# Optimization experiments

Hardware: AMD Instinct MI355X
Metric: run time of the kernel (lower is better)

Reference implementation:

```python
import jax, jax.numpy as jnp
import numpy as np

# Module constants (from init_kwargs + mp_num=8 from the mesh)
D_MODEL = 1024
N_HEAD = 16
D_HEAD = 64
D_ROT = 64
MP = 8
B, S = 2, 2048
LOCAL = N_HEAD * D_HEAD // MP          # 128 : per-mp-shard qkv dim
F_IN = N_HEAD * D_HEAD * 3 + D_MODEL * 8  # 11264 : fused qkv+ff projection width
D_OUT_IN = D_MODEL + 4 * D_MODEL       # 5120 : attn (1024) + glu (4096) into output_proj
LN_EPS = 1e-5


def _rotate_every_two(x):
    # x: [..., d] with d even -> interleaved (-x2, x1)
    x1 = x[..., ::2]
    x2 = x[..., 1::2]
    return jnp.stack((-x2, x1), axis=-1).reshape(*x.shape[:-1], -1)


def _fixed_pos_embedding(seq_len, dim):
    inv_freq = 1.0 / (10000.0 ** (np.arange(0, dim, 2) / dim))
    t = np.einsum('i,j->ij', np.arange(seq_len), inv_freq)  # [S, dim//2]
    return jnp.asarray(np.sin(t), jnp.float32), jnp.asarray(np.cos(t), jnp.float32)


def _apply_rotary(x, sin, cos):
    # x: [B, S, mp, D_ROT]; sin/cos: [S, D_ROT//2]
    sin = jnp.repeat(sin, 2, axis=-1)[-x.shape[-3]:, None, :]  # [S,1,D_ROT]
    cos = jnp.repeat(cos, 2, axis=-1)[-x.shape[-3]:, None, :]
    return x * cos + _rotate_every_two(x) * sin


def setup_inputs() -> dict:
    key = jax.random.key(0)
    ks = jax.random.split(key, 4)
    x = jax.random.normal(ks[0], (B, S, D_MODEL), jnp.float32)
    attn_bias = jnp.zeros((1, S, S), jnp.float32)
    ln_scale = jnp.ones((D_MODEL,), jnp.float32)
    ln_offset = jnp.zeros((D_MODEL,), jnp.float32)
    w_in = jax.random.normal(ks[1], (D_MODEL, F_IN), jnp.float32) / np.sqrt(D_MODEL)
    b_in = jnp.zeros((F_IN,), jnp.float32)
    w_out = jax.random.normal(ks[2], (D_OUT_IN, D_MODEL), jnp.float32) / np.sqrt(D_MODEL)
    b_out = jnp.zeros((D_MODEL,), jnp.float32)
    return {"x": x, "attn_bias": attn_bias, "ln_scale": ln_scale, "ln_offset": ln_offset,
            "w_in": w_in, "b_in": b_in, "w_out": w_out, "b_out": b_out}


def reference(x, attn_bias, ln_scale, ln_offset, w_in, b_in, w_out, b_out):
    b, s, d = x.shape
    # LayerNorm (create_scale=True, create_offset=True, eps=1e-5)
    mu = jnp.mean(x, axis=-1, keepdims=True)
    var = jnp.var(x, axis=-1, keepdims=True)
    h = (x - mu) * jax.lax.rsqrt(var + LN_EPS) * ln_scale + ln_offset
    # fused QKV + FF projection, then mp split: [B,S,mp,F_IN/mp]
    proj = (h @ w_in + b_in).reshape(b, s, MP, -1)
    q, v, k, ff = jnp.split(proj, [LOCAL, 2 * LOCAL, 3 * LOCAL], axis=-1)
    # rotary on the first D_ROT dims of each mp shard (head_split is a shape no-op)
    sin, cos = _fixed_pos_embedding(s, D_ROT)
    q = jnp.concatenate([_apply_rotary(q[..., :D_ROT], sin, cos), q[..., D_ROT:]], axis=-1)
    k = jnp.concatenate([_apply_rotary(k[..., :D_ROT], sin, cos), k[..., D_ROT:]], axis=-1)
    # attention over h=mp shard-heads of dim LOCAL; scaled by sqrt(d_head) per source
    scale = np.sqrt(D_HEAD).astype(x.dtype)
    logits = jnp.einsum('bthd,bThd->bhtT', q, k) / scale  # [B,MP,S,S]
    causal = jnp.tril(jnp.ones((s, s), x.dtype))[None]
    bias = -1e10 * (1.0 - causal) + attn_bias
    weights = jax.nn.softmax(logits + bias, axis=-1)
    attn_vec = jnp.einsum('bhtT,bThd->bthd', weights, v)  # [B,S,MP,LOCAL]
    # GLU FFN (jax.nn.gelu default = tanh approximation, as in source)
    ff_out, ff_gate = jnp.split(ff, 2, axis=-1)
    glu = ff_out * jax.nn.gelu(ff_gate)  # [B,S,MP,4*D_MODEL/MP]
    # output: concat per-shard then flatten -> output_proj
    out = jnp.concatenate([attn_vec, glu], axis=-1).reshape(b, s, -1)  # [B,S,5120]
    return out @ w_out + b_out
```

## Files before the change

kernel.cpp:

```cpp
#include <hip/hip_runtime.h>
#include <stdint.h>

#define B_   2
#define S_   2048
#define DM   1024
#define FIN  11264
#define DOUT 5120
#define NSH  8
#define DH   128
#define ROWS (B_*S_)

typedef __attribute__((ext_vector_type(8))) __bf16 bf16x8;
typedef __attribute__((ext_vector_type(4))) __bf16 bf16x4;
typedef __attribute__((ext_vector_type(4))) float  f32x4;

union U2 { unsigned int u; __bf16 h[2]; };

__device__ __forceinline__ void gload16(const void* g, void* l) {
    __builtin_amdgcn_global_load_lds((const __attribute__((address_space(1))) void*)g,
                                     (__attribute__((address_space(3))) void*)l, 16, 0, 0);
}

__global__ __launch_bounds__(256) void ln_kernel(const float* __restrict__ x,
                                                 const float* __restrict__ sc,
                                                 const float* __restrict__ of,
                                                 __bf16* __restrict__ h) {
    int row = blockIdx.x, t = threadIdx.x;
    const float4 v = *(const float4*)&x[(size_t)row*DM + t*4];
    float s  = v.x + v.y + v.z + v.w;
    float ss = v.x*v.x + v.y*v.y + v.z*v.z + v.w*v.w;
#pragma unroll
    for (int off = 32; off >= 1; off >>= 1) {
        s  += __shfl_xor(s, off);
        ss += __shfl_xor(ss, off);
    }
    __shared__ float rs_[4], rss_[4];
    int wid = t >> 6, lane = t & 63;
    if (lane == 0) { rs_[wid] = s; rss_[wid] = ss; }
    __syncthreads();
    s  = rs_[0] + rs_[1] + rs_[2] + rs_[3];
    ss = rss_[0] + rss_[1] + rss_[2] + rss_[3];
    float mu  = s * (1.f/DM);
    float var = ss * (1.f/DM) - mu*mu;
    float r   = rsqrtf(var + 1e-5f);
    float4 scv = *(const float4*)&sc[t*4];
    float4 ofv = *(const float4*)&of[t*4];
    bf16x4 o;
    o[0] = (__bf16)((v.x-mu)*r*scv.x + ofv.x);
    o[1] = (__bf16)((v.y-mu)*r*scv.y + ofv.y);
    o[2] = (__bf16)((v.z-mu)*r*scv.z + ofv.z);
    o[3] = (__bf16)((v.w-mu)*r*scv.w + ofv.w);
    *(bf16x4*)&h[(size_t)row*DM + t*4] = o;
}

__global__ __launch_bounds__(256) void transpose_kernel(const float* __restrict__ in,
                                                        __bf16* __restrict__ out,
                                                        int R, int C) {
    __shared__ __bf16 tile[64][72];
    int c0 = blockIdx.x * 64, r0 = blockIdx.y * 64;
    int t = threadIdx.x;
#pragma unroll
    for (int it = 0; it < 4; ++it) {
        int flat = it*1024 + t*4;
        int rl = flat >> 6, cl = flat & 63;
        float4 v = *(const float4*)&in[(size_t)(r0+rl)*C + c0 + cl];
        tile[rl][cl+0] = (__bf16)v.x;
        tile[rl][cl+1] = (__bf16)v.y;
        tile[rl][cl+2] = (__bf16)v.z;
        tile[rl][cl+3] = (__bf16)v.w;
    }
    __syncthreads();
#pragma unroll
    for (int it = 0; it < 4; ++it) {
        int flat = it*1024 + t*4;
        int cl = flat >> 6, rl = flat & 63;
        bf16x4 o;
#pragma unroll
        for (int j = 0; j < 4; ++j) o[j] = tile[rl+j][cl];
        *(bf16x4*)&out[(size_t)(c0+cl)*R + r0 + rl] = o;
    }
}

__global__ __launch_bounds__(256) void vtrans_kernel(const __bf16* __restrict__ in,
                                                     __bf16* __restrict__ out) {
    __shared__ __bf16 tile[64*72];
    int d0 = blockIdx.x*64, s0 = blockIdx.y*64;
    size_t base = (size_t)blockIdx.z * (size_t)S_ * DH;
    int t = threadIdx.x;
#pragma unroll
    for (int it = 0; it < 2; ++it) {
        int idx = it*2048 + t*8;
        int sl = idx >> 6, dl = idx & 63;
        bf16x8 v = *(const bf16x8*)&in[base + (size_t)(s0+sl)*DH + d0+dl];
        int ch = ((dl>>3) ^ (sl&7) ^ ((sl>>3)&7)) & 7;
        *(bf16x8*)&tile[sl*72 + ch*8] = v;
    }
    __syncthreads();
#pragma unroll
    for (int it = 0; it < 2; ++it) {
        int idx = it*2048 + t*8;
        int dl = idx >> 6, sl = idx & 63;
        bf16x8 o;
#pragma unroll
        for (int j = 0; j < 8; ++j) {
            int r = sl + j;
            int ch = ((dl>>3) ^ (r&7) ^ ((r>>3)&7)) & 7;
            o[j] = tile[r*72 + ch*8 + (dl&7)];
        }
        *(bf16x8*)&out[base + (size_t)(d0+dl)*S_ + s0 + sl] = o;
    }
}

#define MFMA4(ACCI, BN) \
    acc[ACCI][BN] = __builtin_amdgcn_mfma_f32_16x16x32_bf16(a[(ACCI)&3][0], b[BN][0], acc[ACCI][BN],0,0,0); \
    acc[ACCI][BN] = __builtin_amdgcn_mfma_f32_16x16x32_bf16(a[(ACCI)&3][1], b[BN][1], acc[ACCI][BN],0,0,0);

__global__ __launch_bounds__(512, 2) void gemm256_kernel(const __bf16* __restrict__ A,
                                                         const __bf16* __restrict__ BT,
                                                         const float* __restrict__ bias,
                                                         __bf16* __restrict__ Cb,
                                                         float* __restrict__ Cf,
                                                         int M, int N, int K, int klen) {
    __shared__ __align__(16) char lds[131072];
    int t = threadIdx.x, wid = t >> 6, lane = t & 63;
    int wr = wid >> 2, wc = wid & 3;
    int fr = lane & 15, fq = lane >> 4;
    int kbeg = blockIdx.z * klen;
    int nbx = gridDim.x;
    int bid = blockIdx.y * nbx + blockIdx.x;
    int cpx = (nbx * gridDim.y) >> 3;
    int swz = (bid & 7) * cpx + (bid >> 3);
    int bx = swz % nbx, by = swz / nbx;
    int m0 = by * 256, n0 = bx * 256;

    const __bf16* srcA[4];
    const __bf16* srcB[4];
#pragma unroll
    for (int j = 0; j < 4; ++j) {
        int F = (j*512 + t) * 16;
        int lr = F >> 7, c = (F & 127) ^ ((lr & 7) << 4);
        srcA[j] = A + (size_t)(m0 + lr) * K + kbeg + (c >> 1);
        int row = ((lr >> 5) & 3) * 64 + (lr >> 7) * 32 + (lr & 31);
        srcB[j] = BT + (size_t)(n0 + row) * K + kbeg + (c >> 1);
    }
    int lrAlo[4], lrAhi[4], lrB[4];
#pragma unroll
    for (int i = 0; i < 4; ++i) {
        lrAlo[i] = (wr*128 + i*16 + fr) * 128;
        lrAhi[i] = lrAlo[i] + 64*128;
    }
#pragma unroll
    for (int n = 0; n < 4; ++n)
        lrB[n] = ((n >> 1)*128 + wc*32 + (n & 1)*16 + fr) * 128;
    int swzb = (fr & 7) << 4;
    int cb00 = (fq*16) ^ swzb;
    int cb01 = (64 + fq*16) ^ swzb;

    f32x4 acc[8][4] = {};
    gload16(srcA[0], lds +     0 + wid*1024);
    gload16(srcA[2], lds + 16384 + wid*1024);
    gload16(srcB[0], lds + 32768 + wid*1024);
    gload16(srcB[1], lds + 40960 + wid*1024);
    gload16(srcB[2], lds + 49152 + wid*1024);
    gload16(srcB[3], lds + 57344 + wid*1024);
    gload16(srcA[1], lds +  8192 + wid*1024);
    gload16(srcA[3], lds + 24576 + wid*1024);
    asm volatile("s_waitcnt vmcnt(4)" ::: "memory");
    __builtin_amdgcn_s_barrier();

    int nit = klen >> 6;
    for (int it = 0; it < nit; ++it) {
        const char* bc = lds + (it & 1) * 65536;
        char* bn = lds + ((it & 1) ^ 1) * 65536;
        const char* bcB = bc + 32768;
        int koff = (it + 1) << 6;
        bool pf = (it + 1 < nit);
        bf16x8 a[4][2], b[4][2];
#pragma unroll
        for (int i = 0; i < 4; ++i) {
            a[i][0] = *(const bf16x8*)(bc + lrAlo[i] + cb00);
            a[i][1] = *(const bf16x8*)(bc + lrAlo[i] + cb01);
        }
        b[0][0] = *(const bf16x8*)(bcB + lrB[0] + cb00);
        b[0][1] = *(const bf16x8*)(bcB + lrB[0] + cb01);
        b[1][0] = *(const bf16x8*)(bcB + lrB[1] + cb00);
        b[1][1] = *(const bf16x8*)(bcB + lrB[1] + cb01);
        if (pf) {
            gload16(srcA[0] + koff, bn +     0 + wid*1024);
            gload16(srcA[2] + koff, bn + 16384 + wid*1024);
            gload16(srcB[0] + koff, bn + 32768 + wid*1024);
            gload16(srcB[1] + koff, bn + 40960 + wid*1024);
            gload16(srcB[2] + koff, bn + 49152 + wid*1024);
            gload16(srcB[3] + koff, bn + 57344 + wid*1024);
            gload16(srcA[1] + koff, bn +  8192 + wid*1024);
            gload16(srcA[3] + koff, bn + 24576 + wid*1024);
        }
        __builtin_amdgcn_s_setprio(1);
#pragma unroll
        for (int i = 0; i < 4; ++i) { MFMA4(i,0) MFMA4(i,1) }
        __builtin_amdgcn_s_setprio(0);
        if (pf) asm volatile("s_waitcnt vmcnt(10)" ::: "memory");
        else    asm volatile("s_waitcnt vmcnt(2)" ::: "memory");
        __builtin_amdgcn_s_barrier();
        b[2][0] = *(const bf16x8*)(bcB + lrB[2] + cb00);
        b[2][1] = *(const bf16x8*)(bcB + lrB[2] + cb01);
        b[3][0] = *(const bf16x8*)(bcB + lrB[3] + cb00);
        b[3][1] = *(const bf16x8*)(bcB + lrB[3] + cb01);
        __builtin_amdgcn_s_setprio(1);
#pragma unroll
        for (int i = 0; i < 4; ++i) { MFMA4(i,2) MFMA4(i,3) }
        __builtin_amdgcn_s_setprio(0);
        if (pf) asm volatile("s_waitcnt vmcnt(8)" ::: "memory");
        else    asm volatile("s_waitcnt vmcnt(0)" ::: "memory");
        __builtin_amdgcn_s_barrier();
#pragma unroll
        for (int i = 0; i < 4; ++i) {
            a[i][0] = *(const bf16x8*)(bc + lrAhi[i] + cb00);
            a[i][1] = *(const bf16x8*)(bc + lrAhi[i] + cb01);
        }
        __builtin_amdgcn_s_setprio(1);
#pragma unroll
        for (int i = 0; i < 4; ++i) { MFMA4(4+i,0) MFMA4(4+i,1) MFMA4(4+i,2) MFMA4(4+i,3) }
        __builtin_amdgcn_s_setprio(0);
        if (pf) {
            asm volatile("s_waitcnt vmcnt(4)" ::: "memory");
            __builtin_amdgcn_s_barrier();
        }
    }
    if (Cb) {
#pragma unroll
        for (int i = 0; i < 8; ++i)
#pragma unroll
            for (int n = 0; n < 4; ++n) {
                int col = n0 + wc*64 + (n >> 1)*32 + (n & 1)*16 + fr;
                float bv = bias[col];
#pragma unroll
                for (int r = 0; r < 4; ++r) {
                    int row = m0 + wr*128 + i*16 + fq*4 + r;
                    Cb[(size_t)row*N + col] = (__bf16)(acc[i][n][r] + bv);
                }
            }
    } else {
        float* Cz = Cf + (size_t)blockIdx.z * M * N;
#pragma unroll
        for (int i = 0; i < 8; ++i)
#pragma unroll
            for (int n = 0; n < 4; ++n) {
                int col = n0 + wc*64 + (n >> 1)*32 + (n & 1)*16 + fr;
#pragma unroll
                for (int r = 0; r < 4; ++r) {
                    int row = m0 + wr*128 + i*16 + fq*4 + r;
                    Cz[(size_t)row*N + col] = acc[i][n][r];
                }
            }
    }
}

__global__ __launch_bounds__(256) void addbias_kernel(const float* __restrict__ pk,
                                                      const float* __restrict__ bias,
                                                      float* __restrict__ out) {
    int idx = blockIdx.x * 256 + threadIdx.x;
    const size_t stride = (size_t)ROWS * DM / 4;
    float4 a0 = ((const float4*)pk)[idx];
    float4 a1 = ((const float4*)pk)[idx + stride];
    float4 a2 = ((const float4*)pk)[idx + 2*stride];
    float4 a3 = ((const float4*)pk)[idx + 3*stride];
    float4 bb = ((const float4*)bias)[idx & 255];
    float4 o;
    o.x = a0.x + a1.x + a2.x + a3.x + bb.x;
    o.y = a0.y + a1.y + a2.y + a3.y + bb.y;
    o.z = a0.z + a1.z + a2.z + a3.z + bb.z;
    o.w = a0.w + a1.w + a2.w + a3.w + bb.w;
    ((float4*)out)[idx] = o;
}

__global__ __launch_bounds__(256) void qkv_rope_kernel(const __bf16* __restrict__ proj,
                                                       __bf16* __restrict__ qh,
                                                       __bf16* __restrict__ kh,
                                                       __bf16* __restrict__ vh) {
    int idx = blockIdx.x * 256 + threadIdx.x;
    int i   = idx & 63;
    int p   = (idx >> 6) & 7;
    int row = idx >> 9;
    int s   = row & (S_ - 1);
    int b   = row >> 11;
    const __bf16* base = proj + (size_t)row*FIN + p*1408;
    int d0 = i*2;
    U2 uq, uv, uk;
    uq.u = *(const unsigned int*)&base[d0];
    uv.u = *(const unsigned int*)&base[128+d0];
    uk.u = *(const unsigned int*)&base[256+d0];
    float q0 = uq.h[0], q1 = uq.h[1];
    float v0 = uv.h[0], v1 = uv.h[1];
    float k0 = uk.h[0], k1 = uk.h[1];
    if (d0 < 64) {
        float inv = exp2f(-(float)i * 0.4152410118609203f);
        float ang = (float)s * inv;
        float cn = __cosf(ang), sn = __sinf(ang);
        float a;
        a = q0*cn - q1*sn; q1 = q1*cn + q0*sn; q0 = a;
        a = k0*cn - k1*sn; k1 = k1*cn + k0*sn; k0 = a;
    }
    size_t o = ((size_t)((b*NSH + p)*S_ + s))*DH + d0;
    U2 oq, ok, ov;
    oq.h[0] = (__bf16)(q0*0.125f); oq.h[1] = (__bf16)(q1*0.125f);
    ok.h[0] = (__bf16)k0;          ok.h[1] = (__bf16)k1;
    ov.h[0] = (__bf16)v0;          ov.h[1] = (__bf16)v1;
    *(unsigned int*)&qh[o] = oq.u;
    *(unsigned int*)&kh[o] = ok.u;
    *(unsigned int*)&vh[o] = ov.u;
}

__global__ __launch_bounds__(256) void glu_kernel(const __bf16* __restrict__ proj,
                                                  __bf16* __restrict__ ag) {
    int idx = blockIdx.x * 256 + threadIdx.x;
    int j2  = (idx & 255) * 2;
    int p   = (idx >> 8) & 7;
    int row = idx >> 11;
    const __bf16* bp = proj + (size_t)row*FIN + p*1408;
    U2 xo, xg, o;
    xo.u = *(const unsigned int*)&bp[384 + j2];
    xg.u = *(const unsigned int*)&bp[896 + j2];
#pragma unroll
    for (int j = 0; j < 2; ++j) {
        float g = xg.h[j];
        float e2 = __expf(1.5957691216057308f*(g + 0.044715f*g*g*g));
        float gl = g * (1.f - 1.f/(e2 + 1.f));
        o.h[j] = (__bf16)((float)xo.h[j] * gl);
    }
    *(unsigned int*)&ag[(size_t)row*DOUT + p*640 + 128 + j2] = o.u;
}

__device__ __forceinline__ void stage_kv(const __bf16* Kb, const __bf16* Vg,
                                         char* KsB, char* VsB,
                                         int kvbase, int t, int wid) {
#pragma unroll
    for (int j = 0; j < 4; ++j) {
        int F = (j*256 + t)*16;
        int r = F >> 8, c = F & 255;
        gload16(Kb + (size_t)(kvbase + r)*DH + ((c ^ ((r & 7) << 4)) >> 1),
                KsB + j*4096 + (wid << 10));
    }
#pragma unroll
    for (int j = 0; j < 4; ++j) {
        int F = (j*256 + t)*16;
        int r = F >> 7, c = F & 127;
        gload16(Vg + (size_t)r*S_ + kvbase + ((c ^ ((r & 7) << 4)) >> 1),
                VsB + j*4096 + (wid << 10));
    }
}

__global__ __launch_bounds__(256, 2) void attn_kernel(const __bf16* __restrict__ qh,
                                                      const __bf16* __restrict__ kh,
                                                      const __bf16* __restrict__ vt,
                                                      const float* __restrict__ ab,
                                                      __bf16* __restrict__ ag) {
    __shared__ __bf16 Ks[2*8192];
    __shared__ __bf16 Vs[2*8192];
    __shared__ __bf16 Ps[4][16*72];
    int bh = blockIdx.y;
    int b = bh >> 3, hh = bh & 7;
    int xr = blockIdx.x;
    int qb = (xr & 1) ? (31 - (xr >> 1)) : (xr >> 1);
    int q0 = qb * 64;
    int t = threadIdx.x, wid = t >> 6, lane = t & 63;
    int fr = lane & 15, fkb = (lane >> 4) * 16;
    const __bf16* Qb = qh + (size_t)bh * S_ * DH;
    const __bf16* Kb = kh + (size_t)bh * S_ * DH;
    const __bf16* Vg = vt + (size_t)bh * DH * S_;
    bf16x8 qf[4];
#pragma unroll
    for (int kk = 0; kk < 4; ++kk)
        qf[kk] = *(const bf16x8*)&Qb[(size_t)(q0 + wid*16 + fr)*DH + kk*32 + (lane>>4)*8];
    float m[4] = {-3e38f, -3e38f, -3e38f, -3e38f};
    float l[4] = {0.f, 0.f, 0.f, 0.f};
    f32x4 o[8] = {};
    int rowb = q0 + wid*16 + (lane >> 4)*4;
    int nit = qb + 1;
    stage_kv(Kb, Vg, (char*)Ks, (char*)Vs, 0, t, wid);
    for (int it = 0; it < nit; ++it) {
        int kv0 = it * 64, cur = it & 1;
        float abv[4][4];
#pragma unroll
        for (int n = 0; n < 4; ++n)
#pragma unroll
            for (int r = 0; r < 4; ++r)
                abv[n][r] = ab[(size_t)(rowb + r)*S_ + kv0 + n*16 + fr];
        if (it + 1 < nit) {
            stage_kv(Kb, Vg, (char*)Ks + (cur^1)*16384, (char*)Vs + (cur^1)*16384,
                     kv0 + 64, t, wid);
            asm volatile("s_waitcnt vmcnt(8)" ::: "memory");
        } else {
            asm volatile("s_waitcnt vmcnt(0)" ::: "memory");
        }
        __builtin_amdgcn_s_barrier();
        const char* KsC = (const char*)Ks + cur*16384;
        float pv[4][4];
        __builtin_amdgcn_s_setprio(1);
#pragma unroll
        for (int n = 0; n < 4; ++n) {
            f32x4 sacc = {};
#pragma unroll
            for (int kk = 0; kk < 4; ++kk) {
                int row = n*16 + fr;
                int c2 = (kk*64 + fkb) ^ ((fr & 7) << 4);
                bf16x8 kf = *(const bf16x8*)(KsC + row*256 + c2);
                sacc = __builtin_amdgcn_mfma_f32_16x16x32_bf16(qf[kk], kf, sacc, 0, 0, 0);
            }
#pragma unroll
            for (int r = 0; r < 4; ++r) pv[n][r] = sacc[r];
        }
        __builtin_amdgcn_s_setprio(0);
#pragma unroll
        for (int n = 0; n < 4; ++n) {
            int col = kv0 + n*16 + fr;
#pragma unroll
            for (int r = 0; r < 4; ++r)
                pv[n][r] += abv[n][r] + (col <= rowb + r ? 0.f : -1e10f);
        }
        float alpha[4];
#pragma unroll
        for (int r = 0; r < 4; ++r) {
            float mx = fmaxf(fmaxf(pv[0][r], pv[1][r]), fmaxf(pv[2][r], pv[3][r]));
#pragma unroll
            for (int off = 8; off >= 1; off >>= 1) mx = fmaxf(mx, __shfl_xor(mx, off));
            float mn = fmaxf(m[r], mx);
            alpha[r] = __expf(m[r] - mn);
            m[r] = mn;
            float sum = 0.f;
#pragma unroll
            for (int n = 0; n < 4; ++n) { pv[n][r] = __expf(pv[n][r] - mn); sum += pv[n][r]; }
#pragma unroll
            for (int off = 8; off >= 1; off >>= 1) sum += __shfl_xor(sum, off);
            l[r] = l[r]*alpha[r] + sum;
        }
#pragma unroll
        for (int nf = 0; nf < 8; ++nf)
#pragma unroll
            for (int r = 0; r < 4; ++r) o[nf][r] *= alpha[r];
#pragma unroll
        for (int n = 0; n < 4; ++n)
#pragma unroll
            for (int r = 0; r < 4; ++r)
                Ps[wid][((lane >> 4)*4 + r)*72 + n*16 + fr] = (__bf16)pv[n][r];
        asm volatile("s_waitcnt lgkmcnt(0)" ::: "memory");
        __builtin_amdgcn_sched_barrier(0);
        bf16x8 pf[2];
#pragma unroll
        for (int kk = 0; kk < 2; ++kk)
            pf[kk] = *(const bf16x8*)&Ps[wid][fr*72 + kk*32 + (lane>>4)*8];
        const char* VsC = (const char*)Vs + cur*16384;
        __builtin_amdgcn_s_setprio(1);
#pragma unroll
        for (int nf = 0; nf < 8; ++nf) {
#pragma unroll
            for (int kk = 0; kk < 2; ++kk) {
                int row = nf*16 + fr;
                int c2 = (kk*64 + fkb) ^ ((fr & 7) << 4);
                bf16x8 vf = *(const bf16x8*)(VsC + row*128 + c2);
                o[nf] = __builtin_amdgcn_mfma_f32_16x16x32_bf16(pf[kk], vf, o[nf], 0, 0, 0);
            }
        }
        __builtin_amdgcn_s_setprio(0);
        asm volatile("s_waitcnt lgkmcnt(0)" ::: "memory");
        __builtin_amdgcn_sched_barrier(0);
        __builtin_amdgcn_s_barrier();
    }
    int rq = (lane >> 4) * 4;
#pragma unroll
    for (int r = 0; r < 4; ++r) {
        float inv = 1.f / l[r];
#pragma unroll
        for (int nf = 0; nf < 8; ++nf) {
            int qr = q0 + wid*16 + rq + r;
            int d = nf*16 + fr;
            ag[((size_t)(b*S_ + qr))*DOUT + hh*640 + d] = (__bf16)(o[nf][r] * inv);
        }
    }
}

extern "C" void kernel_launch(void* const* d_in, const int* in_sizes, int n_in,
                              void* d_out, int out_size, void* d_ws, size_t ws_size,
                              hipStream_t stream) {
    const float* x     = (const float*)d_in[0];
    const float* ab    = (const float*)d_in[1];
    const float* lns   = (const float*)d_in[2];
    const float* lno   = (const float*)d_in[3];
    const float* w_in  = (const float*)d_in[4];
    const float* b_in  = (const float*)d_in[5];
    const float* w_out = (const float*)d_in[6];
    const float* b_out = (const float*)d_in[7];
    float* out = (float*)d_out;
    char* ws = (char*)d_ws;

    __bf16* w_in_t  = (__bf16*)(ws);
    __bf16* w_out_t = (__bf16*)(ws +  23068672);
    __bf16* hbuf    = (__bf16*)(ws +  33554432);
    __bf16* proj    = (__bf16*)(ws +  41943040);
    __bf16* vtb     = (__bf16*)(ws +  41943040);
    float*  pk      = (float*)(ws +  52428800);
    __bf16* qh      = (__bf16*)(ws + 134217728);
    __bf16* kh      = (__bf16*)(ws + 142606336);
    __bf16* vh      = (__bf16*)(ws + 150994944);
    __bf16* agb     = (__bf16*)(ws + 159383552);

    transpose_kernel<<<dim3(FIN/64, DM/64), 256, 0, stream>>>(w_in, w_in_t, DM, FIN);
    transpose_kernel<<<dim3(DM/64, DOUT/64), 256, 0, stream>>>(w_out, w_out_t, DOUT, DM);
    ln_kernel<<<ROWS, 256, 0, stream>>>(x, lns, lno, hbuf);
    gemm256_kernel<<<dim3(FIN/256, ROWS/256, 1), 512, 0, stream>>>(hbuf, w_in_t, b_in,
                                                                   proj, nullptr,
                                                                   ROWS, FIN, DM, DM);
    qkv_rope_kernel<<<(ROWS*8*64)/256, 256, 0, stream>>>(proj, qh, kh, vh);
    glu_kernel<<<(ROWS*8*256)/256, 256, 0, stream>>>(proj, agb);
    vtrans_kernel<<<dim3(DH/64, S_/64, B_*NSH), 256, 0, stream>>>(vh, vtb);
    attn_kernel<<<dim3(S_/64, B_*NSH), 256, 0, stream>>>(qh, kh, vtb, ab, agb);
    gemm256_kernel<<<dim3(DM/256, ROWS/256, 4), 512, 0, stream>>>(agb, w_out_t, nullptr,
                                                                  nullptr, pk,
                                                                  ROWS, DM, DOUT, DOUT/4);
    addbias_kernel<<<ROWS*DM/1024, 256, 0, stream>>>(pk, b_out, out);
}
```

Baseline: 312.3 us.

## Restructure GEMM mainloop to four-stage K=32 LDS ring with prefetch depth two

```diff
diff --git a/kernel.cpp b/kernel.cpp
--- a/kernel.cpp
+++ b/kernel.cpp
@@ -111,10 +111,6 @@
     }
 }
 
-#define MFMA4(ACCI, BN) \
-    acc[ACCI][BN] = __builtin_amdgcn_mfma_f32_16x16x32_bf16(a[(ACCI)&3][0], b[BN][0], acc[ACCI][BN],0,0,0); \
-    acc[ACCI][BN] = __builtin_amdgcn_mfma_f32_16x16x32_bf16(a[(ACCI)&3][1], b[BN][1], acc[ACCI][BN],0,0,0);
-
 __global__ __launch_bounds__(512, 2) void gemm256_kernel(const __bf16* __restrict__ A,
                                                          const __bf16* __restrict__ BT,
                                                          const float* __restrict__ bias,
@@ -133,106 +129,90 @@
     int bx = swz % nbx, by = swz / nbx;
     int m0 = by * 256, n0 = bx * 256;
 
-    const __bf16* srcA[4];
-    const __bf16* srcB[4];
-#pragma unroll
-    for (int j = 0; j < 4; ++j) {
-        int F = (j*512 + t) * 16;
-        int lr = F >> 7, c = (F & 127) ^ ((lr & 7) << 4);
-        srcA[j] = A + (size_t)(m0 + lr) * K + kbeg + (c >> 1);
-        int row = ((lr >> 5) & 3) * 64 + (lr >> 7) * 32 + (lr & 31);
-        srcB[j] = BT + (size_t)(n0 + row) * K + kbeg + (c >> 1);
-    }
-    int lrAlo[4], lrAhi[4], lrB[4];
-#pragma unroll
-    for (int i = 0; i < 4; ++i) {
-        lrAlo[i] = (wr*128 + i*16 + fr) * 128;
-        lrAhi[i] = lrAlo[i] + 64*128;
-    }
-#pragma unroll
-    for (int n = 0; n < 4; ++n)
-        lrB[n] = ((n >> 1)*128 + wc*32 + (n & 1)*16 + fr) * 128;
-    int swzb = (fr & 7) << 4;
-    int cb00 = (fq*16) ^ swzb;
-    int cb01 = (64 + fq*16) ^ swzb;
+    const __bf16* pA[2];
+    const __bf16* pB[2];
+#pragma unroll
+    for (int j = 0; j < 2; ++j) {
+        int F = j*8192 + t*16;
+        int row = F >> 6;
+        int co  = (F & 63) ^ (((F >> 7) & 3) << 4);
+        pA[j] = A  + (size_t)(m0 + row) * K + kbeg + (co >> 1);
+        pB[j] = BT + (size_t)(n0 + row) * K + kbeg + (co >> 1);
+    }
+    int offA[8], offB[4];
+#pragma unroll
+    for (int i = 0; i < 8; ++i) {
+        int row = wr*128 + i*16 + fr;
+        offA[i] = row*64 + ((fq*16) ^ (((row >> 1) & 3) << 4));
+    }
+#pragma unroll
+    for (int n = 0; n < 4; ++n) {
+        int row = wc*64 + n*16 + fr;
+        offB[n] = 16384 + row*64 + ((fq*16) ^ (((row >> 1) & 3) << 4));
+    }
 
     f32x4 acc[8][4] = {};
-    gload16(srcA[0], lds +     0 + wid*1024);
-    gload16(srcA[2], lds + 16384 + wid*1024);
-    gload16(srcB[0], lds + 32768 + wid*1024);
-    gload16(srcB[1], lds + 40960 + wid*1024);
-    gload16(srcB[2], lds + 49152 + wid*1024);
-    gload16(srcB[3], lds + 57344 + wid*1024);
-    gload16(srcA[1], lds +  8192 + wid*1024);
-    gload16(srcA[3], lds + 24576 + wid*1024);
+    gload16(pA[0],      lds +     0 + wid*1024);
+    gload16(pA[1],      lds +  8192 + wid*1024);
+    gload16(pB[0],      lds + 16384 + wid*1024);
+    gload16(pB[1],      lds + 24576 + wid*1024);
+    gload16(pA[0] + 32, lds + 32768 +     0 + wid*1024);
+    gload16(pA[1] + 32, lds + 32768 +  8192 + wid*1024);
+    gload16(pB[0] + 32, lds + 32768 + 16384 + wid*1024);
+    gload16(pB[1] + 32, lds + 32768 + 24576 + wid*1024);
     asm volatile("s_waitcnt vmcnt(4)" ::: "memory");
     __builtin_amdgcn_s_barrier();
 
-    int nit = klen >> 6;
-    for (int it = 0; it < nit; ++it) {
-        const char* bc = lds + (it & 1) * 65536;
-        char* bn = lds + ((it & 1) ^ 1) * 65536;
-        const char* bcB = bc + 32768;
-        int koff = (it + 1) << 6;
-        bool pf = (it + 1 < nit);
-        bf16x8 a[4][2], b[4][2];
-#pragma unroll
-        for (int i = 0; i < 4; ++i) {
-            a[i][0] = *(const bf16x8*)(bc + lrAlo[i] + cb00);
-            a[i][1] = *(const bf16x8*)(bc + lrAlo[i] + cb01);
-        }
-        b[0][0] = *(const bf16x8*)(bcB + lrB[0] + cb00);
-        b[0][1] = *(const bf16x8*)(bcB + lrB[0] + cb01);
-        b[1][0] = *(const bf16x8*)(bcB + lrB[1] + cb00);
-        b[1][1] = *(const bf16x8*)(bcB + lrB[1] + cb01);
+    int NT = klen >> 5;
+    for (int tt = 0; tt < NT; ++tt) {
+        const char* sb = lds + (tt & 3) * 32768;
+        bool pf = (tt + 2 < NT);
+        char* sn = lds + ((tt + 2) & 3) * 32768;
+        int ko = (tt + 2) << 5;
+        bf16x8 a[4], b[4];
+#pragma unroll
+        for (int n = 0; n < 4; ++n) b[n] = *(const bf16x8*)(sb + offB[n]);
+#pragma unroll
+        for (int i = 0; i < 4; ++i) a[i] = *(const bf16x8*)(sb + offA[i]);
         if (pf) {
-            gload16(srcA[0] + koff, bn +     0 + wid*1024);
-            gload16(srcA[2] + koff, bn + 16384 + wid*1024);
-            gload16(srcB[0] + koff, bn + 32768 + wid*1024);
-            gload16(srcB[1] + koff, bn + 40960 + wid*1024);
-            gload16(srcB[2] + koff, bn + 49152 + wid*1024);
-            gload16(srcB[3] + koff, bn + 57344 + wid*1024);
-            gload16(srcA[1] + koff, bn +  8192 + wid*1024);
-            gload16(srcA[3] + koff, bn + 24576 + wid*1024);
-        }
+            gload16(pA[0] + ko, sn +        wid*1024);
+            gload16(pA[1] + ko, sn + 8192 + wid*1024);
+        }
+        __builtin_amdgcn_s_barrier();
+        asm volatile("s_waitcnt lgkmcnt(0)");
         __builtin_amdgcn_s_setprio(1);
 #pragma unroll
-        for (int i = 0; i < 4; ++i) { MFMA4(i,0) MFMA4(i,1) }
+        for (int i = 0; i < 4; ++i)
+#pragma unroll
+            for (int n = 0; n < 4; ++n)
+                acc[i][n] = __builtin_amdgcn_mfma_f32_16x16x32_bf16(a[i], b[n], acc[i][n], 0, 0, 0);
         __builtin_amdgcn_s_setprio(0);
-        if (pf) asm volatile("s_waitcnt vmcnt(10)" ::: "memory");
-        else    asm volatile("s_waitcnt vmcnt(2)" ::: "memory");
         __builtin_amdgcn_s_barrier();
-        b[2][0] = *(const bf16x8*)(bcB + lrB[2] + cb00);
-        b[2][1] = *(const bf16x8*)(bcB + lrB[2] + cb01);
-        b[3][0] = *(const bf16x8*)(bcB + lrB[3] + cb00);
-        b[3][1] = *(const bf16x8*)(bcB + lrB[3] + cb01);
+#pragma unroll
+        for (int i = 0; i < 4; ++i) a[i] = *(const bf16x8*)(sb + offA[4 + i]);
+        if (pf) {
+            gload16(pB[0] + ko, sn + 16384 + wid*1024);
+            gload16(pB[1] + ko, sn + 24576 + wid*1024);
+        }
+        __builtin_amdgcn_s_barrier();
+        asm volatile("s_waitcnt lgkmcnt(0)");
         __builtin_amdgcn_s_setprio(1);
 #pragma unroll
-        for (int i = 0; i < 4; ++i) { MFMA4(i,2) MFMA4(i,3) }
+        for (int i = 0; i < 4; ++i)
+#pragma unroll
+            for (int n = 0; n < 4; ++n)
+                acc[4+i][n] = __builtin_amdgcn_mfma_f32_16x16x32_bf16(a[i], b[n], acc[4+i][n], 0, 0, 0);
         __builtin_amdgcn_s_setprio(0);
-        if (pf) asm volatile("s_waitcnt vmcnt(8)" ::: "memory");
-        else    asm volatile("s_waitcnt vmcnt(0)" ::: "memory");
-        __builtin_amdgcn_s_barrier();
-#pragma unroll
-        for (int i = 0; i < 4; ++i) {
-            a[i][0] = *(const bf16x8*)(bc + lrAhi[i] + cb00);
-            a[i][1] = *(const bf16x8*)(bc + lrAhi[i] + cb01);
-        }
-        __builtin_amdgcn_s_setprio(1);
-#pragma unroll
-        for (int i = 0; i < 4; ++i) { MFMA4(4+i,0) MFMA4(4+i,1) MFMA4(4+i,2) MFMA4(4+i,3) }
-        __builtin_amdgcn_s_setprio(0);
-        if (pf) {
-            asm volatile("s_waitcnt vmcnt(4)" ::: "memory");
-            __builtin_amdgcn_s_barrier();
-        }
+        if (pf)               asm volatile("s_waitcnt vmcnt(4)" ::: "memory");
+        else if (tt + 1 < NT) asm volatile("s_waitcnt vmcnt(0)" ::: "memory");
+        if (tt + 1 < NT) __builtin_amdgcn_s_barrier();
     }
     if (Cb) {
 #pragma unroll
         for (int i = 0; i < 8; ++i)
 #pragma unroll
             for (int n = 0; n < 4; ++n) {
-                int col = n0 + wc*64 + (n >> 1)*32 + (n & 1)*16 + fr;
+                int col = n0 + wc*64 + n*16 + fr;
                 float bv = bias[col];
 #pragma unroll
                 for (int r = 0; r < 4; ++r) {
@@ -246,7 +226,7 @@
         for (int i = 0; i < 8; ++i)
 #pragma unroll
             for (int n = 0; n < 4; ++n) {
-                int col = n0 + wc*64 + (n >> 1)*32 + (n & 1)*16 + fr;
+                int col = n0 + wc*64 + n*16 + fr;
 #pragma unroll
                 for (int r = 0; r < 4; ++r) {
                     int row = m0 + wr*128 + i*16 + fq*4 + r;
```

New measurement: 319.8 us. 1.02x slower.

## Fuse GLU into input GEMM epilogue via weight column permutation; fuse rope with V transpose

Applied to the files above, without the earlier changes.

```diff
diff --git a/kernel.cpp b/kernel.cpp
--- a/kernel.cpp
+++ b/kernel.cpp
@@ -19,6 +19,13 @@
 __device__ __forceinline__ void gload16(const void* g, void* l) {
     __builtin_amdgcn_global_load_lds((const __attribute__((address_space(1))) void*)g,
                                      (__attribute__((address_space(3))) void*)l, 16, 0, 0);
+}
+
+__device__ __forceinline__ int origcol(int c) {
+    if (c < 3072) { int p = c / 384; return p*1408 + (c - p*384); }
+    int q = c - 3072; int p = q >> 10; int w = q & 1023;
+    int a = w >> 5, g = (w >> 4) & 1, u = w & 15;
+    return p*1408 + 384 + g*512 + a*16 + u;
 }
 
 __global__ __launch_bounds__(256) void ln_kernel(const float* __restrict__ x,
@@ -81,34 +88,38 @@
     }
 }
 
-__global__ __launch_bounds__(256) void vtrans_kernel(const __bf16* __restrict__ in,
-                                                     __bf16* __restrict__ out) {
-    __shared__ __bf16 tile[64*72];
-    int d0 = blockIdx.x*64, s0 = blockIdx.y*64;
-    size_t base = (size_t)blockIdx.z * (size_t)S_ * DH;
+__global__ __launch_bounds__(256) void transpose_perm_kernel(const float* __restrict__ in,
+                                                             __bf16* __restrict__ out) {
+    __shared__ __bf16 tile[64][72];
+    int c0 = blockIdx.x * 64, r0 = blockIdx.y * 64;
     int t = threadIdx.x;
 #pragma unroll
-    for (int it = 0; it < 2; ++it) {
-        int idx = it*2048 + t*8;
-        int sl = idx >> 6, dl = idx & 63;
-        bf16x8 v = *(const bf16x8*)&in[base + (size_t)(s0+sl)*DH + d0+dl];
-        int ch = ((dl>>3) ^ (sl&7) ^ ((sl>>3)&7)) & 7;
-        *(bf16x8*)&tile[sl*72 + ch*8] = v;
+    for (int it = 0; it < 4; ++it) {
+        int flat = it*1024 + t*4;
+        int rl = flat >> 6, cl = flat & 63;
+        int oc = origcol(c0 + cl);
+        float4 v = *(const float4*)&in[(size_t)(r0+rl)*FIN + oc];
+        tile[rl][cl+0] = (__bf16)v.x;
+        tile[rl][cl+1] = (__bf16)v.y;
+        tile[rl][cl+2] = (__bf16)v.z;
+        tile[rl][cl+3] = (__bf16)v.w;
     }
     __syncthreads();
 #pragma unroll
-    for (int it = 0; it < 2; ++it) {
-        int idx = it*2048 + t*8;
-        int dl = idx >> 6, sl = idx & 63;
-        bf16x8 o;
-#pragma unroll
-        for (int j = 0; j < 8; ++j) {
-            int r = sl + j;
-            int ch = ((dl>>3) ^ (r&7) ^ ((r>>3)&7)) & 7;
-            o[j] = tile[r*72 + ch*8 + (dl&7)];
-        }
-        *(bf16x8*)&out[base + (size_t)(d0+dl)*S_ + s0 + sl] = o;
-    }
+    for (int it = 0; it < 4; ++it) {
+        int flat = it*1024 + t*4;
+        int cl = flat >> 6, rl = flat & 63;
+        bf16x4 o;
+#pragma unroll
+        for (int j = 0; j < 4; ++j) o[j] = tile[rl+j][cl];
+        *(bf16x4*)&out[(size_t)(c0+cl)*DM + r0 + rl] = o;
+    }
+}
+
+__global__ __launch_bounds__(256) void permbias_kernel(const float* __restrict__ b_in,
+                                                       float* __restrict__ bp) {
+    int c = blockIdx.x * 256 + threadIdx.x;
+    if (c < FIN) bp[c] = b_in[origcol(c)];
 }
 
 #define MFMA4(ACCI, BN) \
@@ -118,7 +129,8 @@
 __global__ __launch_bounds__(512, 2) void gemm256_kernel(const __bf16* __restrict__ A,
                                                          const __bf16* __restrict__ BT,
                                                          const float* __restrict__ bias,
-                                                         __bf16* __restrict__ Cb,
+                                                         __bf16* __restrict__ Cqvk,
+                                                         __bf16* __restrict__ Cglu,
                                                          float* __restrict__ Cf,
                                                          int M, int N, int K, int klen) {
     __shared__ __align__(16) char lds[131072];
@@ -227,20 +239,7 @@
             __builtin_amdgcn_s_barrier();
         }
     }
-    if (Cb) {
-#pragma unroll
-        for (int i = 0; i < 8; ++i)
-#pragma unroll
-            for (int n = 0; n < 4; ++n) {
-                int col = n0 + wc*64 + (n >> 1)*32 + (n & 1)*16 + fr;
-                float bv = bias[col];
-#pragma unroll
-                for (int r = 0; r < 4; ++r) {
-                    int row = m0 + wr*128 + i*16 + fq*4 + r;
-                    Cb[(size_t)row*N + col] = (__bf16)(acc[i][n][r] + bv);
-                }
-            }
-    } else {
+    if (Cf) {
         float* Cz = Cf + (size_t)blockIdx.z * M * N;
 #pragma unroll
         for (int i = 0; i < 8; ++i)
@@ -253,6 +252,41 @@
                     Cz[(size_t)row*N + col] = acc[i][n][r];
                 }
             }
+    } else if (n0 < 3072) {
+#pragma unroll
+        for (int i = 0; i < 8; ++i)
+#pragma unroll
+            for (int n = 0; n < 4; ++n) {
+                int col = n0 + wc*64 + (n >> 1)*32 + (n & 1)*16 + fr;
+                float bv = bias[col];
+#pragma unroll
+                for (int r = 0; r < 4; ++r) {
+                    int row = m0 + wr*128 + i*16 + fq*4 + r;
+                    Cqvk[(size_t)row*3072 + col] = (__bf16)(acc[i][n][r] + bv);
+                }
+            }
+    } else {
+        int q = n0 - 3072;
+        int p = q >> 10;
+#pragma unroll
+        for (int m = 0; m < 2; ++m) {
+            int off = wc*64 + m*32;
+            float bo = bias[n0 + off + fr];
+            float bg = bias[n0 + off + 16 + fr];
+            int j = (((q & 1023) + off) >> 5) * 16 + fr;
+            int colg = p*640 + 128 + j;
+#pragma unroll
+            for (int i = 0; i < 8; ++i)
+#pragma unroll
+                for (int r = 0; r < 4; ++r) {
+                    int row = m0 + wr*128 + i*16 + fq*4 + r;
+                    float ov = acc[i][2*m][r] + bo;
+                    float gv = acc[i][2*m+1][r] + bg;
+                    float e2 = __expf(1.5957691216057308f*(gv + 0.044715f*gv*gv*gv));
+                    float gl = gv * (1.f - 1.f/(e2 + 1.f));
+                    Cglu[(size_t)row*DOUT + colg] = (__bf16)(ov * gl);
+                }
+        }
     }
 }
 
@@ -274,61 +308,63 @@
     ((float4*)out)[idx] = o;
 }
 
-__global__ __launch_bounds__(256) void qkv_rope_kernel(const __bf16* __restrict__ proj,
-                                                       __bf16* __restrict__ qh,
-                                                       __bf16* __restrict__ kh,
-                                                       __bf16* __restrict__ vh) {
-    int idx = blockIdx.x * 256 + threadIdx.x;
-    int i   = idx & 63;
-    int p   = (idx >> 6) & 7;
-    int row = idx >> 9;
-    int s   = row & (S_ - 1);
-    int b   = row >> 11;
-    const __bf16* base = proj + (size_t)row*FIN + p*1408;
-    int d0 = i*2;
-    U2 uq, uv, uk;
-    uq.u = *(const unsigned int*)&base[d0];
-    uv.u = *(const unsigned int*)&base[128+d0];
-    uk.u = *(const unsigned int*)&base[256+d0];
-    float q0 = uq.h[0], q1 = uq.h[1];
-    float v0 = uv.h[0], v1 = uv.h[1];
-    float k0 = uk.h[0], k1 = uk.h[1];
-    if (d0 < 64) {
-        float inv = exp2f(-(float)i * 0.4152410118609203f);
-        float ang = (float)s * inv;
-        float cn = __cosf(ang), sn = __sinf(ang);
-        float a;
-        a = q0*cn - q1*sn; q1 = q1*cn + q0*sn; q0 = a;
-        a = k0*cn - k1*sn; k1 = k1*cn + k0*sn; k0 = a;
-    }
-    size_t o = ((size_t)((b*NSH + p)*S_ + s))*DH + d0;
-    U2 oq, ok, ov;
-    oq.h[0] = (__bf16)(q0*0.125f); oq.h[1] = (__bf16)(q1*0.125f);
-    ok.h[0] = (__bf16)k0;          ok.h[1] = (__bf16)k1;
-    ov.h[0] = (__bf16)v0;          ov.h[1] = (__bf16)v1;
-    *(unsigned int*)&qh[o] = oq.u;
-    *(unsigned int*)&kh[o] = ok.u;
-    *(unsigned int*)&vh[o] = ov.u;
-}
-
-__global__ __launch_bounds__(256) void glu_kernel(const __bf16* __restrict__ proj,
-                                                  __bf16* __restrict__ ag) {
-    int idx = blockIdx.x * 256 + threadIdx.x;
-    int j2  = (idx & 255) * 2;
-    int p   = (idx >> 8) & 7;
-    int row = idx >> 11;
-    const __bf16* bp = proj + (size_t)row*FIN + p*1408;
-    U2 xo, xg, o;
-    xo.u = *(const unsigned int*)&bp[384 + j2];
-    xg.u = *(const unsigned int*)&bp[896 + j2];
-#pragma unroll
-    for (int j = 0; j < 2; ++j) {
-        float g = xg.h[j];
-        float e2 = __expf(1.5957691216057308f*(g + 0.044715f*g*g*g));
-        float gl = g * (1.f - 1.f/(e2 + 1.f));
-        o.h[j] = (__bf16)((float)xo.h[j] * gl);
-    }
-    *(unsigned int*)&ag[(size_t)row*DOUT + p*640 + 128 + j2] = o.u;
+__global__ __launch_bounds__(256) void rqkv_kernel(const __bf16* __restrict__ proj2,
+                                                   __bf16* __restrict__ qh,
+                                                   __bf16* __restrict__ kh,
+                                                   __bf16* __restrict__ vt) {
+    __shared__ __bf16 tile[64*144];
+    int r0 = blockIdx.x * 64;
+    int p  = blockIdx.y;
+    int t  = threadIdx.x;
+    int b  = r0 >> 11;
+    int bh = b*NSH + p;
+#pragma unroll
+    for (int j = 0; j < 4; ++j) {
+        int e = (j*256 + t) * 8;
+        int sl = e >> 7, d = e & 127;
+        const __bf16* rowp = proj2 + (size_t)(r0 + sl)*3072 + p*384;
+        bf16x8 vq = *(const bf16x8*)&rowp[d];
+        bf16x8 vv = *(const bf16x8*)&rowp[128 + d];
+        bf16x8 vk = *(const bf16x8*)&rowp[256 + d];
+        int s = (r0 + sl) & (S_ - 1);
+        if (d < 64) {
+#pragma unroll
+            for (int u = 0; u < 4; ++u) {
+                int i = (d >> 1) + u;
+                float inv = exp2f(-(float)i * 0.4152410118609203f);
+                float ang = (float)s * inv;
+                float cn = __cosf(ang), sn = __sinf(ang);
+                float q0 = vq[2*u], q1 = vq[2*u+1];
+                float k0 = vk[2*u], k1 = vk[2*u+1];
+                vq[2*u]   = (__bf16)(q0*cn - q1*sn);
+                vq[2*u+1] = (__bf16)(q1*cn + q0*sn);
+                vk[2*u]   = (__bf16)(k0*cn - k1*sn);
+                vk[2*u+1] = (__bf16)(k1*cn + k0*sn);
+            }
+        }
+#pragma unroll
+        for (int u = 0; u < 8; ++u) vq[u] = (__bf16)((float)vq[u] * 0.125f);
+        size_t o = ((size_t)bh * S_ + s) * DH + d;
+        *(bf16x8*)&qh[o] = vq;
+        *(bf16x8*)&kh[o] = vk;
+        int ch = ((d >> 3) + sl) & 15;
+        *(bf16x8*)&tile[sl*144 + ch*8] = vv;
+    }
+    __syncthreads();
+#pragma unroll
+    for (int j = 0; j < 4; ++j) {
+        int e = (j*256 + t) * 8;
+        int d = e >> 6, sb = e & 63;
+        bf16x8 o;
+#pragma unroll
+        for (int u = 0; u < 8; ++u) {
+            int sl = sb + u;
+            int ch = ((d >> 3) + sl) & 15;
+            o[u] = tile[sl*144 + ch*8 + (d & 7)];
+        }
+        size_t ov = ((size_t)bh * DH + d) * S_ + (r0 & (S_ - 1)) + sb;
+        *(bf16x8*)&vt[ov] = o;
+    }
 }
 
 __device__ __forceinline__ void stage_kv(const __bf16* Kb, const __bf16* Vg,
@@ -496,26 +532,25 @@
     __bf16* w_in_t  = (__bf16*)(ws);
     __bf16* w_out_t = (__bf16*)(ws +  23068672);
     __bf16* hbuf    = (__bf16*)(ws +  33554432);
-    __bf16* proj    = (__bf16*)(ws +  41943040);
-    __bf16* vtb     = (__bf16*)(ws +  41943040);
-    float*  pk      = (float*)(ws +  52428800);
-    __bf16* qh      = (__bf16*)(ws + 134217728);
-    __bf16* kh      = (__bf16*)(ws + 142606336);
-    __bf16* vh      = (__bf16*)(ws + 150994944);
-    __bf16* agb     = (__bf16*)(ws + 159383552);
-
-    transpose_kernel<<<dim3(FIN/64, DM/64), 256, 0, stream>>>(w_in, w_in_t, DM, FIN);
+    __bf16* proj2   = (__bf16*)(ws +  41943040);
+    __bf16* vtb     = (__bf16*)(ws +  67108864);
+    __bf16* qh      = (__bf16*)(ws +  75497472);
+    __bf16* kh      = (__bf16*)(ws +  83886080);
+    __bf16* agb     = (__bf16*)(ws +  92274688);
+    float*  pk      = (float*)(ws + 134217728);
+    float*  bperm   = (float*)(ws + 134217728);
+
+    transpose_perm_kernel<<<dim3(FIN/64, DM/64), 256, 0, stream>>>(w_in, w_in_t);
     transpose_kernel<<<dim3(DM/64, DOUT/64), 256, 0, stream>>>(w_out, w_out_t, DOUT, DM);
+    permbias_kernel<<<(FIN + 255)/256, 256, 0, stream>>>(b_in, bperm);
     ln_kernel<<<ROWS, 256, 0, stream>>>(x, lns, lno, hbuf);
-    gemm256_kernel<<<dim3(FIN/256, ROWS/256, 1), 512, 0, stream>>>(hbuf, w_in_t, b_in,
-                                                                   proj, nullptr,
+    gemm256_kernel<<<dim3(FIN/256, ROWS/256, 1), 512, 0, stream>>>(hbuf, w_in_t, bperm,
+                                                                   proj2, agb, nullptr,
                                                                    ROWS, FIN, DM, DM);
-    qkv_rope_kernel<<<(ROWS*8*64)/256, 256, 0, stream>>>(proj, qh, kh, vh);
-    glu_kernel<<<(ROWS*8*256)/256, 256, 0, stream>>>(proj, agb);
-    vtrans_kernel<<<dim3(DH/64, S_/64, B_*NSH), 256, 0, stream>>>(vh, vtb);
+    rqkv_kernel<<<dim3(ROWS/64, NSH), 256, 0, stream>>>(proj2, qh, kh, vtb);
     attn_kernel<<<dim3(S_/64, B_*NSH), 256, 0, stream>>>(qh, kh, vtb, ab, agb);
     gemm256_kernel<<<dim3(DM/256, ROWS/256, 4), 512, 0, stream>>>(agb, w_out_t, nullptr,
-                                                                  nullptr, pk,
+                                                                  nullptr, nullptr, pk,
                                                                   ROWS, DM, DOUT, DOUT/4);
     addbias_kernel<<<ROWS*DM/1024, 256, 0, stream>>>(pk, b_out, out);
 }
```

New measurement: 292.6 us. 1.07x faster.
